# Performance work log

Measured on AMD Instinct MI355X. Metric: run time of the kernel, lower is better.

## Reference

```python
import jax, jax.numpy as jnp
import numpy as np
from jax import lax

B, CIN, L, COUT, K = 64, 64, 4096, 128, 7
STRIDE, PAD = 1, 3
POOL, POOL_STRIDE = 2, 2
BN_EPS = 1e-5


def setup_inputs() -> dict:
    key = jax.random.key(0)
    ks = jax.random.split(key, 7)
    I = jax.random.normal(ks[0], (B, CIN, L), jnp.float32)
    bn_gamma = 1.0 + 0.1 * jax.random.normal(ks[1], (CIN,), jnp.float32)
    bn_beta = 0.1 * jax.random.normal(ks[2], (CIN,), jnp.float32)
    bn_mean = 0.1 * jax.random.normal(ks[3], (CIN,), jnp.float32)
    bn_var = jax.random.uniform(ks[4], (CIN,), jnp.float32, 0.5, 1.5)
    conv_w = 0.05 * jax.random.normal(ks[5], (COUT, CIN, K), jnp.float32)
    # XNOR-Net style per-output-channel scale alpha = mean(|W|) over (Cin, K)
    alpha = jnp.mean(jnp.abs(conv_w), axis=(1, 2))  # [COUT]
    prelu_w = jnp.full((1,), 0.25, jnp.float32)  # nn.PReLU() default: 1 shared param
    return dict(I=I, bn_gamma=bn_gamma, bn_beta=bn_beta, bn_mean=bn_mean,
                bn_var=bn_var, conv_w=conv_w, alpha=alpha, prelu_w=prelu_w)


def reference(I, bn_gamma, bn_beta, bn_mean, bn_var, conv_w, alpha, prelu_w):
    # BatchNorm1d (eval mode: running stats), per-channel over dim 1
    scale = (bn_gamma / jnp.sqrt(bn_var + BN_EPS))[None, :, None]
    x = (I - bn_mean[None, :, None]) * scale + bn_beta[None, :, None]
    # Binarize (sign; sign(0)=0 matches torch.sign)
    x = jnp.sign(x)
    # Conv1d, no bias, zero padding=3, stride=1  -> [B, COUT, L]
    y = lax.conv_general_dilated(x, conv_w, window_strides=(STRIDE,),
                                 padding=[(PAD, PAD)],
                                 dimension_numbers=('NCH', 'OIH', 'NCH'))
    # alpha scale (per output channel)
    y = y * alpha[None, :, None]
    # PReLU with single shared parameter
    y = jnp.where(y > 0, y, prelu_w[0] * y)
    # MaxPool1d(kernel=2, stride=2)
    y = lax.reduce_window(y, -jnp.inf, lax.max,
                          (1, 1, POOL), (1, 1, POOL_STRIDE), 'VALID')
    return y
```

## Files before the change

### kernel.cpp

```cpp
#include <hip/hip_runtime.h>
#include <hip/hip_bf16.h>
#include <stdint.h>

#define BATCH 64
#define CIN   64
#define LEN   4096
#define COUT  128
#define KW    7
#define LPOOL 2048
#define NT    4
#define RROWS 72
#define RAWP  80
#define SPITCH 64

typedef __bf16 v8bf __attribute__((ext_vector_type(8)));
typedef unsigned short v8us __attribute__((ext_vector_type(8)));
typedef float  v4f  __attribute__((ext_vector_type(4)));

typedef const __attribute__((address_space(1))) void* gp1_t;
typedef __attribute__((address_space(3))) void* lp3_t;

__global__ __launch_bounds__(256)
void wconv_kernel(const float* __restrict__ W, ushort* __restrict__ Wt) {
    int i = blockIdx.x * 256 + threadIdx.x;
    if (i >= COUT * CIN * KW) return;
    int co  = i / (CIN * KW);
    int rem = i - co * (CIN * KW);
    int ci  = rem / KW;
    int k   = rem - ci * KW;
    uint u = __float_as_uint(W[i]);
    uint r = (u + 0x7FFFu + ((u >> 16) & 1u)) >> 16;
    Wt[(k * COUT + co) * CIN + ci] = (ushort)r;
}

static __device__ __forceinline__ void sync_lds() {
    asm volatile("s_waitcnt lgkmcnt(0)" ::: "memory");
    __builtin_amdgcn_s_barrier();
}
static __device__ __forceinline__ void wait_vm0() {
    asm volatile("s_waitcnt vmcnt(0)" ::: "memory");
}

__global__ __launch_bounds__(256, 4)
void conv_kernel(const float* __restrict__ I,
                 const float* __restrict__ bn_g, const float* __restrict__ bn_b,
                 const float* __restrict__ bn_m, const float* __restrict__ bn_v,
                 const ushort* __restrict__ Wt,
                 const float* __restrict__ alpha, const float* __restrict__ prelu,
                 float* __restrict__ out) {
    __shared__ __attribute__((aligned(16))) float  raw[CIN * RAWP];
    __shared__ __attribute__((aligned(16))) ushort stg[RROWS * SPITCH];

    int tid = threadIdx.x;
    int lane = tid & 63, wave = tid >> 6;
    int b = blockIdx.y, bx = blockIdx.x;
    int l0base = bx * (64 * NT);

    const float* Ib = I + (size_t)b * CIN * LEN;

    float* rawb = raw + wave * 1280;
    const char* gb[5]; int cb[5];
    #pragma unroll
    for (int i = 0; i < 5; ++i) {
        int m = i * 64 + lane;
        int cil = m / 20;
        int c   = m - 20 * cil;
        cb[i] = 16 * c - 32;
        gb[i] = (const char*)(Ib + (size_t)(16 * wave + cil) * LEN) + cb[i];
    }

    auto dma_tile = [&](int l0t) {
        int l4 = 4 * l0t;
        #pragma unroll
        for (int i = 0; i < 5; ++i) {
            int off = cb[i] + l4;
            if (off >= 0 && off + 16 <= LEN * 4)
                __builtin_amdgcn_global_load_lds((gp1_t)(gb[i] + l4),
                                                 (lp3_t)(rawb + i * 256), 16, 0, 0);
        }
    };

    dma_tile(l0base);

    int oc  = lane & 1;
    int brq = lane >> 1;
    int g8  = 2 * wave + oc;
    float sc[8], mn[8], bt[8];
    if (lane < 36) {
        #pragma unroll
        for (int c = 0; c < 8; ++c) {
            int ci = 8 * g8 + c;
            sc[c] = __fdiv_rn(bn_g[ci], __fsqrt_rn(__fadd_rn(bn_v[ci], 1e-5f)));
            mn[c] = bn_m[ci];
            bt[c] = bn_b[ci];
        }
    }

    int quad = lane >> 4, lr = lane & 15;
    int cout0 = wave * 32;
    const ushort* wbase = Wt + ((size_t)cout0 + lr) * CIN + quad * 8;
    float pw  = prelu[0];
    float al0 = alpha[cout0 + lr];
    float al1 = alpha[cout0 + 16 + lr];
    float* obase = out + ((size_t)b * COUT) * LPOOL + bx * (32 * NT);

    v8bf c00 = *(const v8bf*)(wbase);
    v8bf c01 = *(const v8bf*)(wbase + 16 * CIN);
    v8bf c10 = *(const v8bf*)(wbase + 32);
    v8bf c11 = *(const v8bf*)(wbase + 32 + 16 * CIN);

    auto binarize = [&](int l0t) {
        if (lane < 36) {
            const float4* r4 = (const float4*)rawb;
            float4 fr[8];
            #pragma unroll
            for (int c = 0; c < 8; ++c)
                fr[c] = r4[(8 * oc + c) * 20 + brq + 1];
            #pragma unroll
            for (int j = 0; j < 4; ++j) {
                int r = 4 * brq + j;
                int p = l0t - 4 + r;
                bool pok = (p >= 0) && (p < LEN);
                v8us u;
                #pragma unroll
                for (int c = 0; c < 8; ++c) {
                    float v = ((const float*)&fr[c])[j];
                    float x = __fadd_rn(__fmul_rn(__fsub_rn(v, mn[c]), sc[c]), bt[c]);
                    ushort s = x > 0.f ? (ushort)0x3F80 : (x < 0.f ? (ushort)0xBF80 : (ushort)0);
                    u[c] = pok ? s : (ushort)0;
                }
                *(v8us*)(&stg[r * SPITCH + ((g8 ^ (r & 7)) << 3)]) = u;
            }
        }
    };

    wait_vm0();
    binarize(l0base);
    sync_lds();

    for (int t = 0; t < NT; ++t) {
        int l0 = l0base + t * 64;

        v4f acc[4][2];
        #pragma unroll
        for (int mt = 0; mt < 4; ++mt) { acc[mt][0] = (v4f)0.f; acc[mt][1] = (v4f)0.f; }

        #pragma unroll 1
        for (int k = 0; k < KW; ++k) {
            int nk = (k == KW - 1) ? 0 : k + 1;
            const ushort* wn = wbase + nk * COUT * CIN;
            v8bf n00 = *(const v8bf*)(wn);
            v8bf n01 = *(const v8bf*)(wn + 16 * CIN);
            v8bf n10 = *(const v8bf*)(wn + 32);
            v8bf n11 = *(const v8bf*)(wn + 32 + 16 * CIN);

            int rk = lr + 1 + k;
            int s8 = rk & 7;
            const ushort* a0p = &stg[rk * SPITCH + ((quad ^ s8) << 3)];
            const ushort* a1p = &stg[rk * SPITCH + (((quad ^ 4) ^ s8) << 3)];
            #pragma unroll
            for (int mt = 0; mt < 4; ++mt) {
                v8bf a0 = *(const v8bf*)(a0p + mt * 16 * SPITCH);
                v8bf a1 = *(const v8bf*)(a1p + mt * 16 * SPITCH);
                acc[mt][0] = __builtin_amdgcn_mfma_f32_16x16x32_bf16(a0, c00, acc[mt][0], 0, 0, 0);
                acc[mt][1] = __builtin_amdgcn_mfma_f32_16x16x32_bf16(a0, c01, acc[mt][1], 0, 0, 0);
                acc[mt][0] = __builtin_amdgcn_mfma_f32_16x16x32_bf16(a1, c10, acc[mt][0], 0, 0, 0);
                acc[mt][1] = __builtin_amdgcn_mfma_f32_16x16x32_bf16(a1, c11, acc[mt][1], 0, 0, 0);
            }
            c00 = n00; c01 = n01; c10 = n10; c11 = n11;
        }

        if (t + 1 < NT) dma_tile(l0 + 64);

        float pv[2][4][2];
        #pragma unroll
        for (int n2 = 0; n2 < 2; ++n2) {
            float al = n2 ? al1 : al0;
            #pragma unroll
            for (int mt = 0; mt < 4; ++mt) {
                float v0 = acc[mt][n2][0] * al; v0 = v0 > 0.f ? v0 : pw * v0;
                float v1 = acc[mt][n2][1] * al; v1 = v1 > 0.f ? v1 : pw * v1;
                float v2 = acc[mt][n2][2] * al; v2 = v2 > 0.f ? v2 : pw * v2;
                float v3 = acc[mt][n2][3] * al; v3 = v3 > 0.f ? v3 : pw * v3;
                pv[n2][mt][0] = fmaxf(v0, v1);
                pv[n2][mt][1] = fmaxf(v2, v3);
            }
        }
        float* ob = obase + t * 32;
        #pragma unroll
        for (int n2 = 0; n2 < 2; ++n2) {
            int co = cout0 + n2 * 16 + lr;
            float* ocp = ob + (size_t)co * LPOOL + quad * 2;
            #pragma unroll
            for (int mt = 0; mt < 4; ++mt)
                *(float2*)(ocp + mt * 8) = make_float2(pv[n2][mt][0], pv[n2][mt][1]);
        }

        if (t + 1 < NT) {
            sync_lds();
            wait_vm0();
            binarize(l0 + 64);
            sync_lds();
        }
    }
}

extern "C" void kernel_launch(void* const* d_in, const int* in_sizes, int n_in,
                              void* d_out, int out_size, void* d_ws, size_t ws_size,
                              hipStream_t stream) {
    const float* I      = (const float*)d_in[0];
    const float* bn_g   = (const float*)d_in[1];
    const float* bn_b   = (const float*)d_in[2];
    const float* bn_m   = (const float*)d_in[3];
    const float* bn_v   = (const float*)d_in[4];
    const float* conv_w = (const float*)d_in[5];
    const float* alpha  = (const float*)d_in[6];
    const float* prelu  = (const float*)d_in[7];
    float* out = (float*)d_out;

    ushort* Wt = (ushort*)d_ws;

    wconv_kernel<<<(COUT * CIN * KW + 255) / 256, 256, 0, stream>>>(conv_w, Wt);
    dim3 grid(LEN / (64 * NT), BATCH);
    conv_kernel<<<grid, 256, 0, stream>>>(I, bn_g, bn_b, bn_m, bn_v, Wt, alpha, prelu, out);
}
```

Measured before the change: 179.1 us.

## Switch to single 128-position tile per block with 2x2 wave tiling

Replaces the per-block loop over four 64-position tiles, which used a DMA/binarize/compute pipeline, with one 128-position tile per block. The raw fp32 input and the bf16 staging buffer now share aliased LDS, and the tile is loaded in a single global_load_lds pass. Waves are arranged 2x2 over positions and output channels, so each wave computes 64 channels and reuses each activation fragment across four MFMAs. This cuts cross-tile synchronisation and halo reloading and raises reuse per LDS read. In exchange the grid has more, shorter blocks, the launch bound drops to 3 blocks per SM, and there is no overlap between load and compute inside a block.

```diff
diff --git a/kernel.cpp b/kernel.cpp
--- a/kernel.cpp
+++ b/kernel.cpp
@@ -8,9 +8,9 @@
 #define COUT  128
 #define KW    7
 #define LPOOL 2048
-#define NT    4
-#define RROWS 72
-#define RAWP  80
+#define BL    128
+#define RROWS 136
+#define RAWC  144
 #define SPITCH 64
 
 typedef __bf16 v8bf __attribute__((ext_vector_type(8)));
@@ -41,166 +41,149 @@
     asm volatile("s_waitcnt vmcnt(0)" ::: "memory");
 }
 
-__global__ __launch_bounds__(256, 4)
+__global__ __launch_bounds__(256, 3)
 void conv_kernel(const float* __restrict__ I,
                  const float* __restrict__ bn_g, const float* __restrict__ bn_b,
                  const float* __restrict__ bn_m, const float* __restrict__ bn_v,
                  const ushort* __restrict__ Wt,
                  const float* __restrict__ alpha, const float* __restrict__ prelu,
                  float* __restrict__ out) {
-    __shared__ __attribute__((aligned(16))) float  raw[CIN * RAWP];
-    __shared__ __attribute__((aligned(16))) ushort stg[RROWS * SPITCH];
+    __shared__ __attribute__((aligned(16))) char smem[CIN * RAWC * 4];
+    float*        raw  = (float*)smem;
+    const float4* raw4 = (const float4*)smem;
+    ushort*       stg  = (ushort*)smem;
 
     int tid = threadIdx.x;
     int lane = tid & 63, wave = tid >> 6;
     int b = blockIdx.y, bx = blockIdx.x;
-    int l0base = bx * (64 * NT);
+    int l0 = bx * BL;
 
     const float* Ib = I + (size_t)b * CIN * LEN;
 
-    float* rawb = raw + wave * 1280;
-    const char* gb[5]; int cb[5];
-    #pragma unroll
-    for (int i = 0; i < 5; ++i) {
-        int m = i * 64 + lane;
-        int cil = m / 20;
-        int c   = m - 20 * cil;
-        cb[i] = 16 * c - 32;
-        gb[i] = (const char*)(Ib + (size_t)(16 * wave + cil) * LEN) + cb[i];
-    }
-
-    auto dma_tile = [&](int l0t) {
-        int l4 = 4 * l0t;
-        #pragma unroll
-        for (int i = 0; i < 5; ++i) {
-            int off = cb[i] + l4;
-            if (off >= 0 && off + 16 <= LEN * 4)
-                __builtin_amdgcn_global_load_lds((gp1_t)(gb[i] + l4),
-                                                 (lp3_t)(rawb + i * 256), 16, 0, 0);
-        }
-    };
-
-    dma_tile(l0base);
-
-    int oc  = lane & 1;
-    int brq = lane >> 1;
-    int g8  = 2 * wave + oc;
+    #pragma unroll
+    for (int i = 0; i < 9; ++i) {
+        int s  = wave * 9 + i;
+        int n  = s * 64 + lane;
+        int ci = n / 36;
+        int c  = n - 36 * ci;
+        int off = 16 * c - 32 + 4 * l0;
+        if (off >= 0 && off + 16 <= LEN * 4)
+            __builtin_amdgcn_global_load_lds((gp1_t)((const char*)(Ib + (size_t)ci * LEN) + off),
+                                             (lp3_t)(raw + s * 256), 16, 0, 0);
+    }
+
+    int oc = lane & 1, quadA = lane >> 1;
+    int o  = 2 * wave + oc;
     float sc[8], mn[8], bt[8];
-    if (lane < 36) {
-        #pragma unroll
-        for (int c = 0; c < 8; ++c) {
-            int ci = 8 * g8 + c;
-            sc[c] = __fdiv_rn(bn_g[ci], __fsqrt_rn(__fadd_rn(bn_v[ci], 1e-5f)));
-            mn[c] = bn_m[ci];
-            bt[c] = bn_b[ci];
-        }
+    #pragma unroll
+    for (int c = 0; c < 8; ++c) {
+        int ci = 8 * o + c;
+        sc[c] = __fdiv_rn(bn_g[ci], __fsqrt_rn(__fadd_rn(bn_v[ci], 1e-5f)));
+        mn[c] = bn_m[ci];
+        bt[c] = bn_b[ci];
     }
 
     int quad = lane >> 4, lr = lane & 15;
-    int cout0 = wave * 32;
-    const ushort* wbase = Wt + ((size_t)cout0 + lr) * CIN + quad * 8;
-    float pw  = prelu[0];
-    float al0 = alpha[cout0 + lr];
-    float al1 = alpha[cout0 + 16 + lr];
-    float* obase = out + ((size_t)b * COUT) * LPOOL + bx * (32 * NT);
-
-    v8bf c00 = *(const v8bf*)(wbase);
-    v8bf c01 = *(const v8bf*)(wbase + 16 * CIN);
-    v8bf c10 = *(const v8bf*)(wbase + 32);
-    v8bf c11 = *(const v8bf*)(wbase + 32 + 16 * CIN);
-
-    auto binarize = [&](int l0t) {
-        if (lane < 36) {
-            const float4* r4 = (const float4*)rawb;
-            float4 fr[8];
+    int wl = wave >> 1, wc = wave & 1;
+    float pw = prelu[0];
+    float al[4];
+    #pragma unroll
+    for (int n2 = 0; n2 < 4; ++n2) al[n2] = alpha[64 * wc + 16 * n2 + lr];
+
+    wait_vm0();
+
+    float4 fr[8], fr2[8];
+    bool two = (lane < 4);
+    int quad2 = 32 + (lane >> 1);
+    #pragma unroll
+    for (int c = 0; c < 8; ++c)
+        fr[c] = raw4[(8 * o + c) * 36 + quadA + 1];
+    if (two) {
+        #pragma unroll
+        for (int c = 0; c < 8; ++c)
+            fr2[c] = raw4[(8 * o + c) * 36 + quad2 + 1];
+    }
+    sync_lds();
+
+    {
+        #pragma unroll
+        for (int j = 0; j < 4; ++j) {
+            int r = 4 * quadA + j;
+            int p = l0 - 4 + r;
+            bool pok = (p >= 0) && (p < LEN);
+            v8us u;
             #pragma unroll
-            for (int c = 0; c < 8; ++c)
-                fr[c] = r4[(8 * oc + c) * 20 + brq + 1];
+            for (int c = 0; c < 8; ++c) {
+                float v = ((const float*)&fr[c])[j];
+                float x = __fadd_rn(__fmul_rn(__fsub_rn(v, mn[c]), sc[c]), bt[c]);
+                ushort s = x > 0.f ? (ushort)0x3F80 : (x < 0.f ? (ushort)0xBF80 : (ushort)0);
+                u[c] = pok ? s : (ushort)0;
+            }
+            *(v8us*)(&stg[r * SPITCH + ((o ^ (r & 7)) << 3)]) = u;
+        }
+        if (two) {
             #pragma unroll
             for (int j = 0; j < 4; ++j) {
-                int r = 4 * brq + j;
-                int p = l0t - 4 + r;
+                int r = 4 * quad2 + j;
+                int p = l0 - 4 + r;
                 bool pok = (p >= 0) && (p < LEN);
                 v8us u;
                 #pragma unroll
                 for (int c = 0; c < 8; ++c) {
-                    float v = ((const float*)&fr[c])[j];
+                    float v = ((const float*)&fr2[c])[j];
                     float x = __fadd_rn(__fmul_rn(__fsub_rn(v, mn[c]), sc[c]), bt[c]);
                     ushort s = x > 0.f ? (ushort)0x3F80 : (x < 0.f ? (ushort)0xBF80 : (ushort)0);
                     u[c] = pok ? s : (ushort)0;
                 }
-                *(v8us*)(&stg[r * SPITCH + ((g8 ^ (r & 7)) << 3)]) = u;
+                *(v8us*)(&stg[r * SPITCH + ((o ^ (r & 7)) << 3)]) = u;
             }
         }
-    };
-
-    wait_vm0();
-    binarize(l0base);
+    }
     sync_lds();
 
-    for (int t = 0; t < NT; ++t) {
-        int l0 = l0base + t * 64;
-
-        v4f acc[4][2];
-        #pragma unroll
-        for (int mt = 0; mt < 4; ++mt) { acc[mt][0] = (v4f)0.f; acc[mt][1] = (v4f)0.f; }
-
-        #pragma unroll 1
-        for (int k = 0; k < KW; ++k) {
-            int nk = (k == KW - 1) ? 0 : k + 1;
-            const ushort* wn = wbase + nk * COUT * CIN;
-            v8bf n00 = *(const v8bf*)(wn);
-            v8bf n01 = *(const v8bf*)(wn + 16 * CIN);
-            v8bf n10 = *(const v8bf*)(wn + 32);
-            v8bf n11 = *(const v8bf*)(wn + 32 + 16 * CIN);
-
-            int rk = lr + 1 + k;
-            int s8 = rk & 7;
-            const ushort* a0p = &stg[rk * SPITCH + ((quad ^ s8) << 3)];
-            const ushort* a1p = &stg[rk * SPITCH + (((quad ^ 4) ^ s8) << 3)];
+    v4f acc[4][4];
+    #pragma unroll
+    for (int mt = 0; mt < 4; ++mt)
+        #pragma unroll
+        for (int n2 = 0; n2 < 4; ++n2) acc[mt][n2] = (v4f)0.f;
+
+    #pragma unroll 1
+    for (int k = 0; k < KW; ++k) {
+        int rbase = 64 * wl + lr + 1 + k;
+        int s8 = (lr + 1 + k) & 7;
+        const ushort* wk = Wt + (size_t)k * (COUT * CIN) + (size_t)(64 * wc + lr) * CIN;
+        #pragma unroll
+        for (int h = 0; h < 2; ++h) {
+            const ushort* wh = wk + h * 32 + quad * 8;
+            v8bf w0 = *(const v8bf*)(wh);
+            v8bf w1 = *(const v8bf*)(wh + 16 * CIN);
+            v8bf w2 = *(const v8bf*)(wh + 32 * CIN);
+            v8bf w3 = *(const v8bf*)(wh + 48 * CIN);
+            const ushort* ap = &stg[rbase * SPITCH + ((quad ^ (h << 2) ^ s8) << 3)];
             #pragma unroll
             for (int mt = 0; mt < 4; ++mt) {
-                v8bf a0 = *(const v8bf*)(a0p + mt * 16 * SPITCH);
-                v8bf a1 = *(const v8bf*)(a1p + mt * 16 * SPITCH);
-                acc[mt][0] = __builtin_amdgcn_mfma_f32_16x16x32_bf16(a0, c00, acc[mt][0], 0, 0, 0);
-                acc[mt][1] = __builtin_amdgcn_mfma_f32_16x16x32_bf16(a0, c01, acc[mt][1], 0, 0, 0);
-                acc[mt][0] = __builtin_amdgcn_mfma_f32_16x16x32_bf16(a1, c10, acc[mt][0], 0, 0, 0);
-                acc[mt][1] = __builtin_amdgcn_mfma_f32_16x16x32_bf16(a1, c11, acc[mt][1], 0, 0, 0);
+                v8bf a = *(const v8bf*)(ap + mt * 16 * SPITCH);
+                acc[mt][0] = __builtin_amdgcn_mfma_f32_16x16x32_bf16(a, w0, acc[mt][0], 0, 0, 0);
+                acc[mt][1] = __builtin_amdgcn_mfma_f32_16x16x32_bf16(a, w1, acc[mt][1], 0, 0, 0);
+                acc[mt][2] = __builtin_amdgcn_mfma_f32_16x16x32_bf16(a, w2, acc[mt][2], 0, 0, 0);
+                acc[mt][3] = __builtin_amdgcn_mfma_f32_16x16x32_bf16(a, w3, acc[mt][3], 0, 0, 0);
             }
-            c00 = n00; c01 = n01; c10 = n10; c11 = n11;
-        }
-
-        if (t + 1 < NT) dma_tile(l0 + 64);
-
-        float pv[2][4][2];
-        #pragma unroll
-        for (int n2 = 0; n2 < 2; ++n2) {
-            float al = n2 ? al1 : al0;
-            #pragma unroll
-            for (int mt = 0; mt < 4; ++mt) {
-                float v0 = acc[mt][n2][0] * al; v0 = v0 > 0.f ? v0 : pw * v0;
-                float v1 = acc[mt][n2][1] * al; v1 = v1 > 0.f ? v1 : pw * v1;
-                float v2 = acc[mt][n2][2] * al; v2 = v2 > 0.f ? v2 : pw * v2;
-                float v3 = acc[mt][n2][3] * al; v3 = v3 > 0.f ? v3 : pw * v3;
-                pv[n2][mt][0] = fmaxf(v0, v1);
-                pv[n2][mt][1] = fmaxf(v2, v3);
-            }
-        }
-        float* ob = obase + t * 32;
-        #pragma unroll
-        for (int n2 = 0; n2 < 2; ++n2) {
-            int co = cout0 + n2 * 16 + lr;
-            float* ocp = ob + (size_t)co * LPOOL + quad * 2;
-            #pragma unroll
-            for (int mt = 0; mt < 4; ++mt)
-                *(float2*)(ocp + mt * 8) = make_float2(pv[n2][mt][0], pv[n2][mt][1]);
-        }
-
-        if (t + 1 < NT) {
-            sync_lds();
-            wait_vm0();
-            binarize(l0 + 64);
-            sync_lds();
+        }
+    }
+
+    #pragma unroll
+    for (int n2 = 0; n2 < 4; ++n2) {
+        int co = 64 * wc + 16 * n2 + lr;
+        float* ocp = out + ((size_t)b * COUT + co) * LPOOL
+                   + (l0 >> 1) + 32 * wl + 2 * quad;
+        float a2 = al[n2];
+        #pragma unroll
+        for (int mt = 0; mt < 4; ++mt) {
+            float v0 = acc[mt][n2][0] * a2; v0 = v0 > 0.f ? v0 : pw * v0;
+            float v1 = acc[mt][n2][1] * a2; v1 = v1 > 0.f ? v1 : pw * v1;
+            float v2 = acc[mt][n2][2] * a2; v2 = v2 > 0.f ? v2 : pw * v2;
+            float v3 = acc[mt][n2][3] * a2; v3 = v3 > 0.f ? v3 : pw * v3;
+            *(float2*)(ocp + 8 * mt) = make_float2(fmaxf(v0, v1), fmaxf(v2, v3));
         }
     }
 }
@@ -221,6 +204,6 @@
     ushort* Wt = (ushort*)d_ws;
 
     wconv_kernel<<<(COUT * CIN * KW + 255) / 256, 256, 0, stream>>>(conv_w, Wt);
-    dim3 grid(LEN / (64 * NT), BATCH);
+    dim3 grid(LEN / BL, BATCH);
     conv_kernel<<<grid, 256, 0, stream>>>(I, bn_g, bn_b, bn_m, bn_v, Wt, alpha, prelu, out);
 }
```

Result: no change. 182.2 us (+1.7%).
